# Kernel tuning notes

Measured on AMD Instinct MI355X. Metric: run time of the kernel, lower is better.

The kernel has to match this reference:

```python
import jax, jax.numpy as jnp
import numpy as np

IN_FEATURES = 4096
OUT_FEATURES = 4096
K = 256
D = 8

def setup_inputs() -> dict:
    key = jax.random.key(0)
    k1, k2, k3 = jax.random.split(key, 3)
    x = jax.random.normal(k1, (4, 2048, IN_FEATURES), dtype=jnp.float32)
    codebook = jax.random.normal(k2, (K, D), dtype=jnp.float16)
    n_codes = OUT_FEATURES * IN_FEATURES // D  # 2,097,152
    indices = jax.random.randint(k3, (n_codes,), 0, K, dtype=jnp.int64)
    return {"x": x, "codebook": codebook, "indices": indices}

def reference(x, codebook, indices):
    orig_dtype = x.dtype
    x_fp16 = x.astype(jnp.float16)
    # Gather codes then reshape into the dense weight [out_features, in_features]
    W_q = codebook[indices].reshape(OUT_FEATURES, IN_FEATURES)  # fp16
    # F.linear: out = x @ W.T
    out = jnp.einsum('bsi,oi->bso', x_fp16, W_q)
    return out.astype(orig_dtype)
```

## Files before the change

### kernel.cpp

```cpp
#include <hip/hip_runtime.h>


typedef _Float16 f16;
typedef _Float16 f16x8 __attribute__((ext_vector_type(8)));
typedef float f32x4 __attribute__((ext_vector_type(4)));

#define KDIM 4096
#define NDIM 4096
#define MDIM 8192

struct Flags { int cb_mode; int x_bf16; int idx64; int pad; };

__device__ inline float bf16_to_f32(unsigned short w) {
    union { unsigned u; float f; } c; c.u = ((unsigned)w) << 16; return c.f;
}
__device__ inline unsigned short f32_to_bf16(float f) {
    union { float f; unsigned u; } c; c.f = f;
    unsigned r = c.u + 0x7FFFu + ((c.u >> 16) & 1u);
    return (unsigned short)(r >> 16);
}


__global__ __launch_bounds__(256) void crom_detect(const unsigned short* __restrict__ cbw,
                                                   const unsigned short* __restrict__ xw,
                                                   const unsigned* __restrict__ idxw,
                                                   Flags* __restrict__ flags) {
    __shared__ int cnt[4];
    const int t = threadIdx.x;
    if (t < 4) cnt[t] = 0;
    __syncthreads();
    int c_cb = 0, c_f32ok = 1, c_x = 0, c_z = 0;
    for (int j = 0; j < 8; ++j) {
        int e5 = (cbw[t * 8 + j] >> 10) & 31;
        c_cb += (e5 == 15) || (e5 == 16);
    }
    const float* cbf = (const float*)cbw;
    for (int j = 0; j < 4; ++j) {
        float v = cbf[t * 4 + j];
        if (!(__builtin_fabsf(v) < 1024.0f)) c_f32ok = 0;
        else { f16 h = (f16)v; if ((float)h != v) c_f32ok = 0; }
    }
    for (int j = 0; j < 8; ++j) {
        int e8 = (xw[t * 8 + j] >> 7) & 255;
        c_x += (e8 >= 115) && (e8 <= 131);
    }
    for (int j = 1; j < 8; j += 2) c_z += (idxw[t * 8 + j] == 0);
    atomicAdd(&cnt[0], c_cb);
    atomicAdd(&cnt[1], c_f32ok);
    atomicAdd(&cnt[2], c_x);
    atomicAdd(&cnt[3], c_z);
    __syncthreads();
    if (t == 0) {
        flags->cb_mode = (cnt[1] == 256) ? 2 : ((cnt[0] > 1300) ? 1 : 0);
        flags->x_bf16  = cnt[2] > 1600;
        flags->idx64   = cnt[3] > 512;
    }
}

__global__ __launch_bounds__(256) void crom_dequant(const void* __restrict__ idxraw,
                                                    const void* __restrict__ cbraw,
                                                    uint4* __restrict__ W,
                                                    const Flags* __restrict__ flags) {
    __shared__ __align__(16) f16 cbL[256 * 8];
    const int t = threadIdx.x;
    const int cb_mode = flags->cb_mode;
    if (cb_mode == 2) {
        const float* cf = (const float*)cbraw;
        f16x8 h;
        for (int j = 0; j < 8; ++j) h[j] = (f16)cf[t * 8 + j];
        *(f16x8*)&cbL[t * 8] = h;
    } else if (cb_mode == 1) {
        const unsigned short* cw = (const unsigned short*)cbraw;
        f16x8 h;
        for (int j = 0; j < 8; ++j) h[j] = (f16)bf16_to_f32(cw[t * 8 + j]);
        *(f16x8*)&cbL[t * 8] = h;
    } else {
        ((uint4*)cbL)[t] = ((const uint4*)cbraw)[t];
    }
    __syncthreads();
    int i = blockIdx.x * 256 + t;
    int code = flags->idx64 ? (int)((const long long*)idxraw)[i]
                            : ((const int*)idxraw)[i];
    W[i] = *(const uint4*)&cbL[code * 8];
}

__global__ __launch_bounds__(256) void crom_cvt_x(const void* __restrict__ X,
                                                  f16x8* __restrict__ Xh,
                                                  const Flags* __restrict__ flags) {
    int i = blockIdx.x * 256 + threadIdx.x;
    f16x8 h;
    if (flags->x_bf16) {
        ushort4 a = ((const ushort4*)X)[2 * i];
        ushort4 b = ((const ushort4*)X)[2 * i + 1];
        h[0] = (f16)bf16_to_f32(a.x); h[1] = (f16)bf16_to_f32(a.y);
        h[2] = (f16)bf16_to_f32(a.z); h[3] = (f16)bf16_to_f32(a.w);
        h[4] = (f16)bf16_to_f32(b.x); h[5] = (f16)bf16_to_f32(b.y);
        h[6] = (f16)bf16_to_f32(b.z); h[7] = (f16)bf16_to_f32(b.w);
    } else {
        float4 a = ((const float4*)X)[2 * i];
        float4 b = ((const float4*)X)[2 * i + 1];
        h[0] = (f16)a.x; h[1] = (f16)a.y; h[2] = (f16)a.z; h[3] = (f16)a.w;
        h[4] = (f16)b.x; h[5] = (f16)b.y; h[6] = (f16)b.z; h[7] = (f16)b.w;
    }
    Xh[i] = h;
}


__device__ __forceinline__ void stage_A(const f16* __restrict__ A, f16* dstbuf,
                                        int m0, int kt, int half, int w, int l) {
#pragma unroll
    for (int it = 0; it < 2; ++it) {
        const int gb = it * 512 + w * 64;
        const int g  = gb + l;
        const int lrl = g >> 3, j = g & 7;
        const int r  = ((lrl >> 6) << 7) + (half << 6) + (lrl & 63);
        const int sc = j ^ (r & 7);
        const f16* src = A + (size_t)(m0 + r) * KDIM + kt * 64 + sc * 8;
        const int lrb = gb >> 3;
        const int rb  = ((lrb >> 6) << 7) + (half << 6) + (lrb & 63);
        __builtin_amdgcn_global_load_lds(
            (const __attribute__((address_space(1))) void*)src,
            (__attribute__((address_space(3))) void*)(dstbuf + rb * 64), 16, 0, 0);
    }
}

__device__ __forceinline__ void stage_B(const f16* __restrict__ B, f16* dstbuf,
                                        int n0, int kt, int half, int w, int l) {
#pragma unroll
    for (int it = 0; it < 2; ++it) {
        const int gb = it * 512 + w * 64;
        const int g  = gb + l;
        const int lrl = g >> 3, j = g & 7;
        const int r  = ((lrl >> 5) << 6) + (half << 5) + (lrl & 31);
        const int sc = j ^ (r & 7);
        const f16* src = B + (size_t)(n0 + r) * KDIM + kt * 64 + sc * 8;
        const int lrb = gb >> 3;
        const int rb  = ((lrb >> 5) << 6) + (half << 5) + (lrb & 31);
        __builtin_amdgcn_global_load_lds(
            (const __attribute__((address_space(1))) void*)src,
            (__attribute__((address_space(3))) void*)(dstbuf + rb * 64), 16, 0, 0);
    }
}

#define VMW(n) do { asm volatile("s_waitcnt vmcnt(" #n ")" ::: "memory"); \
                    __builtin_amdgcn_sched_barrier(0); } while (0)

#define LOAD_AF(Asb, QM)                                                      \
    _Pragma("unroll")                                                         \
    for (int mt = 0; mt < 4; ++mt) {                                          \
        const int ro = (arow + (QM) * 64 + mt * 16) * 64;                     \
        af[mt][0] = *(const f16x8*)&(Asb)[ro + c0];                           \
        af[mt][1] = *(const f16x8*)&(Asb)[ro + c1];                           \
    }

#define LOAD_BF(Bsb, QN, bfx)                                                 \
    _Pragma("unroll")                                                         \
    for (int nt = 0; nt < 2; ++nt) {                                          \
        const int ro = (brow + (QN) * 32 + nt * 16) * 64;                     \
        bfx[nt][0] = *(const f16x8*)&(Bsb)[ro + c0];                          \
        bfx[nt][1] = *(const f16x8*)&(Bsb)[ro + c1];                          \
    }

#define MFMA16(QM, QN, bfx)                                                   \
    _Pragma("unroll")                                                         \
    for (int ks = 0; ks < 2; ++ks)                                            \
        _Pragma("unroll")                                                     \
        for (int mt = 0; mt < 4; ++mt)                                        \
            _Pragma("unroll")                                                 \
            for (int nt = 0; nt < 2; ++nt)                                    \
                acc[(QM) * 4 + mt][(QN) * 2 + nt] =                           \
                    __builtin_amdgcn_mfma_f32_16x16x32_f16(                   \
                        af[mt][ks], bfx[nt][ks],                              \
                        acc[(QM) * 4 + mt][(QN) * 2 + nt], 0, 0, 0);

#define BAR_MFMA(QM, QN, bfx, TAIL)                                           \
    __builtin_amdgcn_s_barrier();                                             \
    asm volatile("s_waitcnt lgkmcnt(0)" ::: "memory");                        \
    __builtin_amdgcn_sched_barrier(0);                                        \
    __builtin_amdgcn_s_setprio(1);                                            \
    MFMA16(QM, QN, bfx);                                                      \
    __builtin_amdgcn_s_setprio(0);                                            \
    TAIL;                                                                     \
    __builtin_amdgcn_s_barrier();

__global__ __launch_bounds__(512, 2) void crom_gemm(const f16* __restrict__ A,
                                                    const f16* __restrict__ B,
                                                    void* __restrict__ Cout,
                                                    const Flags* __restrict__ flags) {
    __shared__ __align__(16) f16 As[2][256 * 64];
    __shared__ __align__(16) f16 Bs[2][256 * 64];

    const int tid  = threadIdx.x;
    const int w    = tid >> 6;
    const int l    = tid & 63;
    const int quad = l >> 4;
    const int lr   = l & 15;
    const int wm   = w >> 2;
    const int wn   = w & 3;

    const int bid = blockIdx.x;
    const int swz = (bid & 7) * 64 + (bid >> 3);
    const int m0  = (swz >> 4) * 256;
    const int n0  = (swz & 15) * 256;

    const int c0 = (quad ^ (lr & 7)) * 8;
    const int c1 = ((4 + quad) ^ (lr & 7)) * 8;
    const int arow = wm * 128 + lr;
    const int brow = wn * 64 + lr;

    f32x4 acc[8][4] = {};
    f16x8 af[4][2], bf0[2][2], bf1[2][2];

    stage_A(A, As[0], m0, 0, 0, w, l);
    stage_A(A, As[0], m0, 0, 1, w, l);
    stage_B(B, Bs[0], n0, 0, 0, w, l);
    stage_B(B, Bs[0], n0, 0, 1, w, l);
    stage_A(A, As[1], m0, 1, 0, w, l);
    stage_B(B, Bs[1], n0, 1, 0, w, l);
    VMW(4);
    __builtin_amdgcn_s_barrier();

    for (int i = 0; i < 31; ++i) {
        const int t0 = 2 * i;
        LOAD_AF(As[0], 0); LOAD_BF(Bs[0], 0, bf0);
        stage_A(A, As[1], m0, t0 + 1, 1, w, l);
        BAR_MFMA(0, 0, bf0, );
        LOAD_BF(Bs[0], 1, bf1);
        stage_B(B, Bs[1], n0, t0 + 1, 1, w, l);
        BAR_MFMA(0, 1, bf1, );
        LOAD_AF(As[0], 1);
        stage_A(A, As[0], m0, t0 + 2, 0, w, l);
        BAR_MFMA(1, 0, bf0, );
        stage_B(B, Bs[0], n0, t0 + 2, 0, w, l);
        BAR_MFMA(1, 1, bf1, VMW(4));
        LOAD_AF(As[1], 0); LOAD_BF(Bs[1], 0, bf0);
        stage_A(A, As[0], m0, t0 + 2, 1, w, l);
        BAR_MFMA(0, 0, bf0, );
        LOAD_BF(Bs[1], 1, bf1);
        stage_B(B, Bs[0], n0, t0 + 2, 1, w, l);
        BAR_MFMA(0, 1, bf1, );
        LOAD_AF(As[1], 1);
        stage_A(A, As[1], m0, t0 + 3, 0, w, l);
        BAR_MFMA(1, 0, bf0, );
        stage_B(B, Bs[1], n0, t0 + 3, 0, w, l);
        BAR_MFMA(1, 1, bf1, VMW(4));
    }

    LOAD_AF(As[0], 0); LOAD_BF(Bs[0], 0, bf0);
    stage_A(A, As[1], m0, 63, 1, w, l);
    BAR_MFMA(0, 0, bf0, );
    LOAD_BF(Bs[0], 1, bf1);
    stage_B(B, Bs[1], n0, 63, 1, w, l);
    BAR_MFMA(0, 1, bf1, );
    LOAD_AF(As[0], 1);
    BAR_MFMA(1, 0, bf0, );
    BAR_MFMA(1, 1, bf1, VMW(0));
    LOAD_AF(As[1], 0); LOAD_BF(Bs[1], 0, bf0);
    BAR_MFMA(0, 0, bf0, );
    LOAD_BF(Bs[1], 1, bf1);
    BAR_MFMA(0, 1, bf1, );
    LOAD_AF(As[1], 1);
    BAR_MFMA(1, 0, bf0, );
    BAR_MFMA(1, 1, bf1, );

    const int out_bf16 = flags->x_bf16;
    if (out_bf16) {
        unsigned short* Cb = (unsigned short*)Cout;
#pragma unroll
        for (int mt = 0; mt < 8; ++mt)
#pragma unroll
            for (int nt = 0; nt < 4; ++nt) {
                const int colg = n0 + wn * 64 + nt * 16 + lr;
#pragma unroll
                for (int r = 0; r < 4; ++r) {
                    const int rowg = m0 + wm * 128 + mt * 16 + quad * 4 + r;
                    Cb[(size_t)rowg * NDIM + colg] = f32_to_bf16(acc[mt][nt][r]);
                }
            }
    } else {
        float* Cf = (float*)Cout;
#pragma unroll
        for (int mt = 0; mt < 8; ++mt)
#pragma unroll
            for (int nt = 0; nt < 4; ++nt) {
                const int colg = n0 + wn * 64 + nt * 16 + lr;
#pragma unroll
                for (int r = 0; r < 4; ++r) {
                    const int rowg = m0 + wm * 128 + mt * 16 + quad * 4 + r;
                    Cf[(size_t)rowg * NDIM + colg] = acc[mt][nt][r];
                }
            }
    }
}


__global__ __launch_bounds__(256) void crom_fused(const void* __restrict__ xraw,
                                                  const void* __restrict__ cbraw,
                                                  const void* __restrict__ idxraw,
                                                  void* __restrict__ outraw) {
    __shared__ __align__(16) f16 cbL[256 * 8];
    __shared__ __align__(16) f16 Asf[128 * 64];
    __shared__ __align__(16) f16 Bsf[128 * 64];
    __shared__ int flagsL[4];

    const int t = threadIdx.x;
    {
        int c_cb = 0, c_f32ok = 1, c_x = 0, c_z = 0;
        const unsigned short* cbw = (const unsigned short*)cbraw;
        for (int j = 0; j < 8; ++j) {
            int e5 = (cbw[t * 8 + j] >> 10) & 31;
            c_cb += (e5 == 15) || (e5 == 16);
        }
        const float* cbf = (const float*)cbraw;
        for (int j = 0; j < 4; ++j) {
            float v = cbf[t * 4 + j];
            if (!(__builtin_fabsf(v) < 1024.0f)) c_f32ok = 0;
            else { f16 h = (f16)v; if ((float)h != v) c_f32ok = 0; }
        }
        const unsigned short* xw = (const unsigned short*)xraw;
        for (int j = 0; j < 8; ++j) {
            int e8 = (xw[t * 8 + j] >> 7) & 255;
            c_x += (e8 >= 115) && (e8 <= 131);
        }
        const unsigned* iw = (const unsigned*)idxraw;
        for (int j = 1; j < 8; j += 2) c_z += (iw[t * 8 + j] == 0);
        if (t < 4) flagsL[t] = 0;
        __syncthreads();
        atomicAdd(&flagsL[0], c_cb);
        atomicAdd(&flagsL[1], c_f32ok);
        atomicAdd(&flagsL[2], c_x);
        atomicAdd(&flagsL[3], c_z);
        __syncthreads();
    }
    const int cb_mode = (flagsL[1] == 256) ? 2 : ((flagsL[0] > 1300) ? 1 : 0);
    const int x_bf16  = flagsL[2] > 1600;
    const int idx64   = flagsL[3] > 512;

    if (cb_mode == 2) {
        const float* cf = (const float*)cbraw;
        f16x8 h;
        for (int j = 0; j < 8; ++j) h[j] = (f16)cf[t * 8 + j];
        *(f16x8*)&cbL[t * 8] = h;
    } else if (cb_mode == 1) {
        const unsigned short* cw = (const unsigned short*)cbraw;
        f16x8 h;
        for (int j = 0; j < 8; ++j) h[j] = (f16)bf16_to_f32(cw[t * 8 + j]);
        *(f16x8*)&cbL[t * 8] = h;
    } else {
        ((uint4*)cbL)[t] = ((const uint4*)cbraw)[t];
    }
    __syncthreads();

    const int m0 = blockIdx.y * 128;
    const int n0 = blockIdx.x * 128;
    const int w = t >> 6, l = t & 63, quad = l >> 4, lr = l & 15;
    const int wm = (w >> 1) * 64, wn = (w & 1) * 64;

    f32x4 acc[4][4] = {};

    for (int kb = 0; kb < KDIM / 64; ++kb) {
        const int k0 = kb * 64;
#pragma unroll
        for (int cc = 0; cc < 4; ++cc) {
            int c = cc * 256 + t, row = c >> 3, j = c & 7;
            int gc = j ^ (row & 7);
            f16x8 h;
            if (!x_bf16) {
                const float4* p = (const float4*)((const float*)xraw +
                                  (size_t)(m0 + row) * KDIM + k0 + gc * 8);
                float4 a = p[0], b = p[1];
                h[0] = (f16)a.x; h[1] = (f16)a.y; h[2] = (f16)a.z; h[3] = (f16)a.w;
                h[4] = (f16)b.x; h[5] = (f16)b.y; h[6] = (f16)b.z; h[7] = (f16)b.w;
            } else {
                const unsigned short* p = (const unsigned short*)xraw +
                                          (size_t)(m0 + row) * KDIM + k0 + gc * 8;
                ushort4 a = *(const ushort4*)p, b = *(const ushort4*)(p + 4);
                h[0] = (f16)bf16_to_f32(a.x); h[1] = (f16)bf16_to_f32(a.y);
                h[2] = (f16)bf16_to_f32(a.z); h[3] = (f16)bf16_to_f32(a.w);
                h[4] = (f16)bf16_to_f32(b.x); h[5] = (f16)bf16_to_f32(b.y);
                h[6] = (f16)bf16_to_f32(b.z); h[7] = (f16)bf16_to_f32(b.w);
            }
            *(f16x8*)&Asf[row * 64 + j * 8] = h;
        }
#pragma unroll
        for (int cc = 0; cc < 4; ++cc) {
            int c = cc * 256 + t, row = c >> 3, j = c & 7;
            int gc = j ^ (row & 7);
            int cpos = (n0 + row) * (KDIM / 8) + kb * 8 + gc;
            int code = idx64 ? (int)((const long long*)idxraw)[cpos]
                             : ((const int*)idxraw)[cpos];
            *(f16x8*)&Bsf[row * 64 + j * 8] = *(const f16x8*)&cbL[code * 8];
        }
        __syncthreads();

#pragma unroll
        for (int ks = 0; ks < 2; ++ks) {
            f16x8 afv[4], bfv[4];
            int gc = ks * 4 + quad;
            int cc2 = gc ^ (lr & 7);
#pragma unroll
            for (int mt = 0; mt < 4; ++mt)
                afv[mt] = *(const f16x8*)&Asf[(wm + mt * 16 + lr) * 64 + cc2 * 8];
#pragma unroll
            for (int nt = 0; nt < 4; ++nt)
                bfv[nt] = *(const f16x8*)&Bsf[(wn + nt * 16 + lr) * 64 + cc2 * 8];
#pragma unroll
            for (int mt = 0; mt < 4; ++mt)
#pragma unroll
                for (int nt = 0; nt < 4; ++nt)
                    acc[mt][nt] = __builtin_amdgcn_mfma_f32_16x16x32_f16(
                        afv[mt], bfv[nt], acc[mt][nt], 0, 0, 0);
        }
        __syncthreads();
    }

    if (x_bf16) {
        unsigned short* Cb = (unsigned short*)outraw;
#pragma unroll
        for (int mt = 0; mt < 4; ++mt)
#pragma unroll
            for (int nt = 0; nt < 4; ++nt) {
                int colg = n0 + wn + nt * 16 + lr;
#pragma unroll
                for (int r = 0; r < 4; ++r) {
                    int rowg = m0 + wm + mt * 16 + quad * 4 + r;
                    Cb[(size_t)rowg * NDIM + colg] = f32_to_bf16(acc[mt][nt][r]);
                }
            }
    } else {
        float* Cf = (float*)outraw;
#pragma unroll
        for (int mt = 0; mt < 4; ++mt)
#pragma unroll
            for (int nt = 0; nt < 4; ++nt) {
                int colg = n0 + wn + nt * 16 + lr;
#pragma unroll
                for (int r = 0; r < 4; ++r) {
                    int rowg = m0 + wm + mt * 16 + quad * 4 + r;
                    Cf[(size_t)rowg * NDIM + colg] = acc[mt][nt][r];
                }
            }
    }
}


extern "C" void kernel_launch(void* const* d_in, const int* in_sizes, int n_in,
                              void* d_out, int out_size, void* d_ws, size_t ws_size,
                              hipStream_t stream) {
    (void)in_sizes; (void)n_in; (void)out_size;
    const void* x   = d_in[0];
    const void* cb  = d_in[1];
    const void* idx = d_in[2];

    const size_t NEED = (size_t)96 * 1024 * 1024 + 4096;

    if (ws_size >= NEED) {
        f16*   Wq    = (f16*)d_ws;
        f16*   Xh    = (f16*)((char*)d_ws + (size_t)32 * 1024 * 1024);
        Flags* flags = (Flags*)((char*)d_ws + (size_t)96 * 1024 * 1024);

        crom_detect<<<1, 256, 0, stream>>>((const unsigned short*)cb,
                                           (const unsigned short*)x,
                                           (const unsigned*)idx, flags);
        crom_dequant<<<2097152 / 256, 256, 0, stream>>>(idx, cb, (uint4*)Wq, flags);
        crom_cvt_x<<<(33554432 / 8) / 256, 256, 0, stream>>>(x, (f16x8*)Xh, flags);
        crom_gemm<<<dim3((MDIM / 256) * (NDIM / 256)), dim3(512), 0, stream>>>(
            Xh, Wq, d_out, flags);
    } else {
        dim3 grid(NDIM / 128, MDIM / 128);
        crom_fused<<<grid, 256, 0, stream>>>(x, cb, idx, d_out);
    }
}
```

Before: 471.5 us.

## Software-pipeline LDS fragment loads across MFMA phases, drop per-phase lgkmcnt wait

Restructures the GEMM main loop so LDS fragment reads for the next phase are issued after the MFMA block of the current phase (and some before it), instead of being issued and waited on with an explicit lgkmcnt(0) before every MFMA burst. Global-to-LDS staging is placed just before the MFMAs inside sched barriers. It also reorders the prologue staging to interleave A and B. This aims to hide LDS read latency behind matrix math, at the cost of more live fragment registers and reliance on compiler-inserted waits for correctness across barriers.

```diff
diff --git a/kernel.cpp b/kernel.cpp
--- a/kernel.cpp
+++ b/kernel.cpp
@@ -173,13 +173,18 @@
                         af[mt][ks], bfx[nt][ks],                              \
                         acc[(QM) * 4 + mt][(QN) * 2 + nt], 0, 0, 0);
 
-#define BAR_MFMA(QM, QN, bfx, TAIL)                                           \
+#define PH(QM, QN, bfx, PRE, STG, POST, TAIL)                                 \
     __builtin_amdgcn_s_barrier();                                             \
-    asm volatile("s_waitcnt lgkmcnt(0)" ::: "memory");                        \
+    __builtin_amdgcn_sched_barrier(0);                                        \
+    PRE;                                                                      \
+    STG;                                                                      \
     __builtin_amdgcn_sched_barrier(0);                                        \
     __builtin_amdgcn_s_setprio(1);                                            \
     MFMA16(QM, QN, bfx);                                                      \
     __builtin_amdgcn_s_setprio(0);                                            \
+    __builtin_amdgcn_sched_barrier(0);                                        \
+    POST;                                                                     \
+    __builtin_amdgcn_sched_barrier(0);                                        \
     TAIL;                                                                     \
     __builtin_amdgcn_s_barrier();
 
@@ -212,56 +217,36 @@
     f16x8 af[4][2], bf0[2][2], bf1[2][2];
 
     stage_A(A, As[0], m0, 0, 0, w, l);
+    stage_B(B, Bs[0], n0, 0, 0, w, l);
     stage_A(A, As[0], m0, 0, 1, w, l);
-    stage_B(B, Bs[0], n0, 0, 0, w, l);
     stage_B(B, Bs[0], n0, 0, 1, w, l);
     stage_A(A, As[1], m0, 1, 0, w, l);
     stage_B(B, Bs[1], n0, 1, 0, w, l);
     VMW(4);
     __builtin_amdgcn_s_barrier();
+    LOAD_AF(As[0], 0);
+    LOAD_BF(Bs[0], 0, bf0);
 
     for (int i = 0; i < 31; ++i) {
         const int t0 = 2 * i;
-        LOAD_AF(As[0], 0); LOAD_BF(Bs[0], 0, bf0);
-        stage_A(A, As[1], m0, t0 + 1, 1, w, l);
-        BAR_MFMA(0, 0, bf0, );
-        LOAD_BF(Bs[0], 1, bf1);
-        stage_B(B, Bs[1], n0, t0 + 1, 1, w, l);
-        BAR_MFMA(0, 1, bf1, );
-        LOAD_AF(As[0], 1);
-        stage_A(A, As[0], m0, t0 + 2, 0, w, l);
-        BAR_MFMA(1, 0, bf0, );
-        stage_B(B, Bs[0], n0, t0 + 2, 0, w, l);
-        BAR_MFMA(1, 1, bf1, VMW(4));
-        LOAD_AF(As[1], 0); LOAD_BF(Bs[1], 0, bf0);
-        stage_A(A, As[0], m0, t0 + 2, 1, w, l);
-        BAR_MFMA(0, 0, bf0, );
-        LOAD_BF(Bs[1], 1, bf1);
-        stage_B(B, Bs[0], n0, t0 + 2, 1, w, l);
-        BAR_MFMA(0, 1, bf1, );
-        LOAD_AF(As[1], 1);
-        stage_A(A, As[1], m0, t0 + 3, 0, w, l);
-        BAR_MFMA(1, 0, bf0, );
-        stage_B(B, Bs[1], n0, t0 + 3, 0, w, l);
-        BAR_MFMA(1, 1, bf1, VMW(4));
-    }
-
-    LOAD_AF(As[0], 0); LOAD_BF(Bs[0], 0, bf0);
-    stage_A(A, As[1], m0, 63, 1, w, l);
-    BAR_MFMA(0, 0, bf0, );
-    LOAD_BF(Bs[0], 1, bf1);
-    stage_B(B, Bs[1], n0, 63, 1, w, l);
-    BAR_MFMA(0, 1, bf1, );
-    LOAD_AF(As[0], 1);
-    BAR_MFMA(1, 0, bf0, );
-    BAR_MFMA(1, 1, bf1, VMW(0));
-    LOAD_AF(As[1], 0); LOAD_BF(Bs[1], 0, bf0);
-    BAR_MFMA(0, 0, bf0, );
-    LOAD_BF(Bs[1], 1, bf1);
-    BAR_MFMA(0, 1, bf1, );
-    LOAD_AF(As[1], 1);
-    BAR_MFMA(1, 0, bf0, );
-    BAR_MFMA(1, 1, bf1, );
+        PH(0, 0, bf0, LOAD_BF(Bs[0], 1, bf1), stage_A(A, As[1], m0, t0 + 1, 1, w, l), , );
+        PH(0, 1, bf1, , stage_B(B, Bs[1], n0, t0 + 1, 1, w, l), LOAD_AF(As[0], 1), VMW(4));
+        PH(1, 0, bf0, , stage_A(A, As[0], m0, t0 + 2, 0, w, l), LOAD_BF(Bs[1], 0, bf0), );
+        PH(1, 1, bf1, , stage_B(B, Bs[0], n0, t0 + 2, 0, w, l), LOAD_AF(As[1], 0), VMW(4));
+        PH(0, 0, bf0, LOAD_BF(Bs[1], 1, bf1), stage_A(A, As[0], m0, t0 + 2, 1, w, l), , );
+        PH(0, 1, bf1, , stage_B(B, Bs[0], n0, t0 + 2, 1, w, l), LOAD_AF(As[1], 1), VMW(4));
+        PH(1, 0, bf0, , stage_A(A, As[1], m0, t0 + 3, 0, w, l), LOAD_BF(Bs[0], 0, bf0), );
+        PH(1, 1, bf1, , stage_B(B, Bs[1], n0, t0 + 3, 0, w, l), LOAD_AF(As[0], 0), VMW(4));
+    }
+
+    PH(0, 0, bf0, LOAD_BF(Bs[0], 1, bf1), stage_A(A, As[1], m0, 63, 1, w, l), , );
+    PH(0, 1, bf1, , stage_B(B, Bs[1], n0, 63, 1, w, l), LOAD_AF(As[0], 1), VMW(4));
+    PH(1, 0, bf0, , , LOAD_BF(Bs[1], 0, bf0), );
+    PH(1, 1, bf1, , , LOAD_AF(As[1], 0), VMW(0));
+    PH(0, 0, bf0, LOAD_BF(Bs[1], 1, bf1), , , );
+    PH(0, 1, bf1, , , LOAD_AF(As[1], 1), );
+    PH(1, 0, bf0, , , , );
+    PH(1, 1, bf1, , , , );
 
     const int out_bf16 = flags->x_bf16;
     if (out_bf16) {
```

After: 513.5 us. +8.9%, slower.
